# Kernel tuning notes

Hardware: AMD Instinct MI355X
Metric: run time of the kernel (lower is better)

Reference implementation:

```python
import jax, jax.numpy as jnp
import numpy as np

N_EMBD = 126
N_HEADS = 6
HEAD_DIM = N_EMBD // N_HEADS  # 21


def setup_inputs() -> dict:
    key = jax.random.key(0)
    k1, k2, k3 = jax.random.split(key, 3)
    B, T = 8, 2048
    x = jax.random.normal(k1, (B, T, N_EMBD), dtype=jnp.float32)
    # torch Linear weights stored as (out, in); we store transposed (in, out) for x @ W
    w_attn = jax.random.normal(k2, (N_EMBD, 3 * N_EMBD), dtype=jnp.float32) * (1.0 / np.sqrt(N_EMBD))
    w_proj = jax.random.normal(k3, (N_EMBD, N_EMBD), dtype=jnp.float32) * (1.0 / np.sqrt(N_EMBD))
    return {"x": x, "w_attn": w_attn, "w_proj": w_proj}


def reference(x, w_attn, w_proj):
    B, T, C = x.shape
    qkv = x @ w_attn                      # [B, T, 3C]
    q, k, v = jnp.split(qkv, 3, axis=-1)  # each [B, T, C]

    def heads(t):  # [B,T,C] -> [B,H,T,hd]
        return t.reshape(B, T, N_HEADS, HEAD_DIM).transpose(0, 2, 1, 3)

    q, k, v = heads(q), heads(k), heads(v)
    scale = 1.0 / np.sqrt(HEAD_DIM).astype(np.float32)
    scores = jnp.einsum('bhqd,bhkd->bhqk', q, k) * scale  # [B,H,T,T]
    causal = jnp.tril(jnp.ones((T, T), dtype=bool))
    scores = jnp.where(causal, scores, jnp.finfo(scores.dtype).min)
    attn = jax.nn.softmax(scores, axis=-1)
    out = jnp.einsum('bhqk,bhkd->bhqd', attn, v)           # [B,H,T,hd]
    out = out.transpose(0, 2, 1, 3).reshape(B, T, C)
    return out @ w_proj
```

## Files before the change

kernel.cpp:

```cpp
#include <hip/hip_runtime.h>
#include <hip/hip_bf16.h>


#define B_ 8
#define T_ 2048
#define C_ 126
#define H_ 6
#define D_ 21
#define TC_ 378
#define KP_ 128
#define DP_ 32
#define M_ 16384
#define QSCALE 0.31481923469333463f

typedef __hip_bfloat16 bf16;
typedef __bf16 bf16_t;
typedef __bf16 bf16x8 __attribute__((ext_vector_type(8)));
typedef float f32x4 __attribute__((ext_vector_type(4)));

__device__ __forceinline__ float ldf(const bf16* p, long i) { return __bfloat162float(p[i]); }
__device__ __forceinline__ float ldf(const float* p, long i) { return p[i]; }
__device__ __forceinline__ void stf(bf16* p, long i, float v) { p[i] = __float2bfloat16(v); }
__device__ __forceinline__ void stf(float* p, long i, float v) { p[i] = v; }

__device__ __forceinline__ unsigned int ld2(const bf16* x, long i) {
  return *(const unsigned int*)((const unsigned short*)x + i);
}
__device__ __forceinline__ unsigned int ld2(const float* x, long i) {
  const float2 f = *(const float2*)(x + i);
  union { bf16_t b[2]; unsigned int u; } cv;
  cv.b[0] = (bf16_t)f.x; cv.b[1] = (bf16_t)f.y;
  return cv.u;
}

__device__ __forceinline__ void probe_dtype(const void* x, int tid, int* sflag) {
  if (tid < 64) {
    const unsigned int w = ((const unsigned int*)x)[tid * 97 + 13];
    const unsigned int e = (w >> 7) & 0xFF;
    const bool bflike = (e >= 115 && e <= 131) || ((w & 0x7FFFu) == 0);
    const unsigned long long mask = __ballot(bflike);
    if (tid == 0) *sflag = (__popcll(mask) >= 40) ? 1 : 0;
  }
  __syncthreads();
}

template <typename T>
__device__ __forceinline__ void prep_w_body(const T* __restrict__ wa,
                                            const T* __restrict__ wp,
                                            bf16_t* __restrict__ WTa,
                                            bf16_t* __restrict__ WTp) {
  const int stride = gridDim.x * blockDim.x;
  const int idx0 = blockIdx.x * blockDim.x + threadIdx.x;
  for (int i = idx0; i < 384 * KP_ + KP_ * KP_; i += stride) {
    if (i < 384 * KP_) {
      const int n = i >> 7, k = i & 127;
      WTa[i] = (k < C_ && n < TC_) ? (bf16_t)ldf(wa, (long)k * TC_ + n) : (bf16_t)0.f;
    } else {
      const int j = i - 384 * KP_;
      const int n = j >> 7, k = j & 127;
      WTp[j] = (k < C_ && n < C_) ? (bf16_t)ldf(wp, (long)k * C_ + n) : (bf16_t)0.f;
    }
  }
}

__global__ __launch_bounds__(256) void prep_w_kernel(
    const void* __restrict__ x, const void* __restrict__ wa,
    const void* __restrict__ wp, bf16_t* __restrict__ WTa,
    bf16_t* __restrict__ WTp) {
  __shared__ int sflag;
  probe_dtype(x, threadIdx.x, &sflag);
  if (sflag) prep_w_body<bf16>((const bf16*)wa, (const bf16*)wp, WTa, WTp);
  else       prep_w_body<float>((const float*)wa, (const float*)wp, WTa, WTp);
}

#define QS_ 40

template <typename T>
__device__ __forceinline__ void qkv_body(
    const T* __restrict__ x, const bf16_t* __restrict__ WT,
    bf16_t* __restrict__ Qb, bf16_t* __restrict__ Kb, bf16_t* __restrict__ VT,
    bf16_t* __restrict__ xs, bf16_t* __restrict__ qbuf,
    bf16_t* __restrict__ kbuf, bf16_t* __restrict__ vbuf) {
  const int m0 = blockIdx.x * 16;
  const int tid = threadIdx.x;
  for (int i = tid; i < 16 * 64; i += 256) {
    const int row = i >> 6, cp = i & 63;
    unsigned int v = 0;
    if (cp < 63) v = ld2(x, (long)(m0 + row) * C_ + 2 * cp);
    ((unsigned int*)xs)[i] = v;
  }
  for (int i = tid; i < 6 * 16 * 11; i += 256) {
    const int h = i / 176, rem = i - h * 176, t = rem / 11, d = 21 + rem % 11;
    qbuf[(h * 16 + t) * QS_ + d] = (bf16_t)0.f;
    kbuf[(h * 16 + t) * QS_ + d] = (bf16_t)0.f;
  }
  for (int i = tid; i < 6 * 11 * 16; i += 256) {
    const int h = i / 176, rem = i - h * 176, d = 21 + rem / 16, t = rem % 16;
    vbuf[(h * 32 + d) * 16 + t] = (d == 21) ? (bf16_t)1.f : (bf16_t)0.f;
  }
  __syncthreads();

  const int wv = tid >> 6, lane = tid & 63;
  const int lr = lane & 15, quad = lane >> 4;
  const bf16_t* ar = xs + lr * KP_ + quad * 8;
  const bf16x8 a0 = *(const bf16x8*)(ar);
  const bf16x8 a1 = *(const bf16x8*)(ar + 32);
  const bf16x8 a2 = *(const bf16x8*)(ar + 64);
  const bf16x8 a3 = *(const bf16x8*)(ar + 96);

  for (int nt = wv; nt < 24; nt += 4) {
    const int n0 = nt * 16;
    const bf16x8* bp = (const bf16x8*)(WT + (long)(n0 + lr) * KP_ + quad * 8);
    f32x4 acc = {0.f, 0.f, 0.f, 0.f};
    acc = __builtin_amdgcn_mfma_f32_16x16x32_bf16(a0, bp[0],  acc, 0, 0, 0);
    acc = __builtin_amdgcn_mfma_f32_16x16x32_bf16(a1, bp[4],  acc, 0, 0, 0);
    acc = __builtin_amdgcn_mfma_f32_16x16x32_bf16(a2, bp[8],  acc, 0, 0, 0);
    acc = __builtin_amdgcn_mfma_f32_16x16x32_bf16(a3, bp[12], acc, 0, 0, 0);

    const int c = n0 + lr;
    if (c < TC_) {
      const int which = c / C_;
      const int cc = c - which * C_;
      const int h = cc / D_, d = cc - h * D_;
#pragma unroll
      for (int r = 0; r < 4; ++r) {
        const int t = quad * 4 + r;
        if (which == 0)
          qbuf[(h * 16 + t) * QS_ + d] = (bf16_t)(acc[r] * QSCALE);
        else if (which == 1)
          kbuf[(h * 16 + t) * QS_ + d] = (bf16_t)acc[r];
        else
          vbuf[(h * 32 + d) * 16 + t] = (bf16_t)acc[r];
      }
    }
  }
  __syncthreads();

  const int b = m0 >> 11, t0 = m0 & 2047;
  for (int i = tid; i < 192; i += 256) {
    const int j = (i < 96) ? i : i - 96;
    const int h = j >> 4, t = j & 15;
    const int4* src = (const int4*)(((i < 96) ? qbuf : kbuf) + (h * 16 + t) * QS_);
    int4* dst = (int4*)((((i < 96) ? Qb : Kb)) + ((long)(b * H_ + h) * T_ + (t0 + t)) * DP_);
    dst[0] = src[0]; dst[1] = src[1]; dst[2] = src[2]; dst[3] = src[3];
  }
  for (int i = tid; i < 192; i += 256) {
    const int h = i >> 5, d = i & 31;
    const int4* src = (const int4*)(vbuf + (h * 32 + d) * 16);
    int4* dst = (int4*)(VT + ((long)(b * H_ + h) * DP_ + d) * T_ + t0);
    dst[0] = src[0]; dst[1] = src[1];
  }
}

__global__ __launch_bounds__(256) void qkv_mfma(
    const void* __restrict__ x, const bf16_t* __restrict__ WT,
    bf16_t* __restrict__ Qb, bf16_t* __restrict__ Kb, bf16_t* __restrict__ VT) {
  __shared__ __align__(16) bf16_t xs[16 * KP_];
  __shared__ __align__(16) bf16_t qbuf[6 * 16 * QS_];
  __shared__ __align__(16) bf16_t kbuf[6 * 16 * QS_];
  __shared__ __align__(16) bf16_t vbuf[6 * 32 * 16];
  __shared__ int sflag;
  probe_dtype(x, threadIdx.x, &sflag);
  if (sflag) qkv_body<bf16>((const bf16*)x, WT, Qb, Kb, VT, xs, qbuf, kbuf, vbuf);
  else       qkv_body<float>((const float*)x, WT, Qb, Kb, VT, xs, qbuf, kbuf, vbuf);
}

__global__ __launch_bounds__(256, 4) void attn_mfma(
    const bf16_t* __restrict__ Qb, const bf16_t* __restrict__ Kb,
    const bf16_t* __restrict__ VT, bf16_t* __restrict__ ATTp) {
  __shared__ __align__(16) float smem[4352];
  const int bh = blockIdx.x;
  const int pr = 63 - blockIdx.y;
  const int tid = threadIdx.x;
  const int wv = tid >> 6, lane = tid & 63;
  const int lr = lane & 15, quad = lane >> 4;
  const int q0 = pr * 32;
  const int mq = quad * 4;

  const bf16_t* Qbh = Qb + (long)bh * T_ * DP_;
  const bf16_t* Kbh = Kb + (long)bh * T_ * DP_;
  const bf16_t* VTbh = VT + (long)bh * DP_ * T_;

  const bf16x8 qf0 = *(const bf16x8*)(Qbh + (long)(q0 + lr) * DP_ + quad * 8);
  const bf16x8 qf1 = *(const bf16x8*)(Qbh + (long)(q0 + 16 + lr) * DP_ + quad * 8);

  f32x4 o00 = {0.f,0.f,0.f,0.f}, o01 = {0.f,0.f,0.f,0.f};
  f32x4 o10 = {0.f,0.f,0.f,0.f}, o11 = {0.f,0.f,0.f,0.f};
  bf16_t* plA0 = (bf16_t*)smem + wv * 2048;
  bf16_t* plA1 = plA0 + 512;
  bf16_t* plB0 = plA0 + 1024;
  bf16_t* plB1 = plA0 + 1536;
  const int rsw = ((lane ^ (lane >> 2)) << 3);
  const int wb0 = ((lr >> 3) << 4) + mq;

  int t = wv;
  for (; t + 4 <= pr; t += 8) {
    const int kbA = t * 32, kbB = (t + 4) * 32;
    const bf16x8 kA0 = *(const bf16x8*)(Kbh + (long)(kbA + lr) * DP_ + quad * 8);
    const bf16x8 kA1 = *(const bf16x8*)(Kbh + (long)(kbA + 16 + lr) * DP_ + quad * 8);
    const bf16x8 kB0 = *(const bf16x8*)(Kbh + (long)(kbB + lr) * DP_ + quad * 8);
    const bf16x8 kB1 = *(const bf16x8*)(Kbh + (long)(kbB + 16 + lr) * DP_ + quad * 8);
    const bf16x8 vA0 = *(const bf16x8*)(VTbh + (long)lr * T_ + kbA + quad * 8);
    const bf16x8 vA1 = *(const bf16x8*)(VTbh + (long)(16 + lr) * T_ + kbA + quad * 8);
    const bf16x8 vB0 = *(const bf16x8*)(VTbh + (long)lr * T_ + kbB + quad * 8);
    const bf16x8 vB1 = *(const bf16x8*)(VTbh + (long)(16 + lr) * T_ + kbB + quad * 8);

    f32x4 sA00 = {0.f,0.f,0.f,0.f}, sA01 = {0.f,0.f,0.f,0.f};
    f32x4 sA10 = {0.f,0.f,0.f,0.f}, sA11 = {0.f,0.f,0.f,0.f};
    f32x4 sB00 = {0.f,0.f,0.f,0.f}, sB01 = {0.f,0.f,0.f,0.f};
    f32x4 sB10 = {0.f,0.f,0.f,0.f}, sB11 = {0.f,0.f,0.f,0.f};
    sA00 = __builtin_amdgcn_mfma_f32_16x16x32_bf16(qf0, kA0, sA00, 0, 0, 0);
    sA01 = __builtin_amdgcn_mfma_f32_16x16x32_bf16(qf0, kA1, sA01, 0, 0, 0);
    sA10 = __builtin_amdgcn_mfma_f32_16x16x32_bf16(qf1, kA0, sA10, 0, 0, 0);
    sA11 = __builtin_amdgcn_mfma_f32_16x16x32_bf16(qf1, kA1, sA11, 0, 0, 0);
    sB00 = __builtin_amdgcn_mfma_f32_16x16x32_bf16(qf0, kB0, sB00, 0, 0, 0);
    sB01 = __builtin_amdgcn_mfma_f32_16x16x32_bf16(qf0, kB1, sB01, 0, 0, 0);
    sB10 = __builtin_amdgcn_mfma_f32_16x16x32_bf16(qf1, kB0, sB10, 0, 0, 0);
    sB11 = __builtin_amdgcn_mfma_f32_16x16x32_bf16(qf1, kB1, sB11, 0, 0, 0);

    if (t + 4 == pr) {
#pragma unroll
      for (int r = 0; r < 4; ++r) {
        if (lr > mq + r) { sB00[r] = -1e30f; sB11[r] = -1e30f; }
        sB01[r] = -1e30f;
      }
    }
#pragma unroll
    for (int r = 0; r < 4; ++r) {
      const int b0 = wb0 + r, b1 = b0 + 32;
      const int i0 = ((b0 ^ (b0 >> 2)) << 3) + (lr & 7);
      const int i1 = ((b1 ^ (b1 >> 2)) << 3) + (lr & 7);
      plA0[i0] = (bf16_t)exp2f(sA00[r]);
      plA0[i1] = (bf16_t)exp2f(sA01[r]);
      plA1[i0] = (bf16_t)exp2f(sA10[r]);
      plA1[i1] = (bf16_t)exp2f(sA11[r]);
      plB0[i0] = (bf16_t)exp2f(sB00[r]);
      plB0[i1] = (bf16_t)exp2f(sB01[r]);
      plB1[i0] = (bf16_t)exp2f(sB10[r]);
      plB1[i1] = (bf16_t)exp2f(sB11[r]);
    }
    __builtin_amdgcn_wave_barrier();
    const bf16x8 pfA0 = *(const bf16x8*)(plA0 + rsw);
    const bf16x8 pfA1 = *(const bf16x8*)(plA1 + rsw);
    const bf16x8 pfB0 = *(const bf16x8*)(plB0 + rsw);
    const bf16x8 pfB1 = *(const bf16x8*)(plB1 + rsw);
    __builtin_amdgcn_wave_barrier();

    o00 = __builtin_amdgcn_mfma_f32_16x16x32_bf16(pfA0, vA0, o00, 0, 0, 0);
    o01 = __builtin_amdgcn_mfma_f32_16x16x32_bf16(pfA0, vA1, o01, 0, 0, 0);
    o10 = __builtin_amdgcn_mfma_f32_16x16x32_bf16(pfA1, vA0, o10, 0, 0, 0);
    o11 = __builtin_amdgcn_mfma_f32_16x16x32_bf16(pfA1, vA1, o11, 0, 0, 0);
    o00 = __builtin_amdgcn_mfma_f32_16x16x32_bf16(pfB0, vB0, o00, 0, 0, 0);
    o01 = __builtin_amdgcn_mfma_f32_16x16x32_bf16(pfB0, vB1, o01, 0, 0, 0);
    o10 = __builtin_amdgcn_mfma_f32_16x16x32_bf16(pfB1, vB0, o10, 0, 0, 0);
    o11 = __builtin_amdgcn_mfma_f32_16x16x32_bf16(pfB1, vB1, o11, 0, 0, 0);
  }

  if (t <= pr) {
    const int kb = t * 32;
    const bf16x8 k0 = *(const bf16x8*)(Kbh + (long)(kb + lr) * DP_ + quad * 8);
    const bf16x8 k1 = *(const bf16x8*)(Kbh + (long)(kb + 16 + lr) * DP_ + quad * 8);
    const bf16x8 v0 = *(const bf16x8*)(VTbh + (long)lr * T_ + kb + quad * 8);
    const bf16x8 v1 = *(const bf16x8*)(VTbh + (long)(16 + lr) * T_ + kb + quad * 8);
    f32x4 s00 = {0.f,0.f,0.f,0.f}, s01 = {0.f,0.f,0.f,0.f};
    f32x4 s10 = {0.f,0.f,0.f,0.f}, s11 = {0.f,0.f,0.f,0.f};
    s00 = __builtin_amdgcn_mfma_f32_16x16x32_bf16(qf0, k0, s00, 0, 0, 0);
    s01 = __builtin_amdgcn_mfma_f32_16x16x32_bf16(qf0, k1, s01, 0, 0, 0);
    s10 = __builtin_amdgcn_mfma_f32_16x16x32_bf16(qf1, k0, s10, 0, 0, 0);
    s11 = __builtin_amdgcn_mfma_f32_16x16x32_bf16(qf1, k1, s11, 0, 0, 0);
    if (t == pr) {
#pragma unroll
      for (int r = 0; r < 4; ++r) {
        if (lr > mq + r) { s00[r] = -1e30f; s11[r] = -1e30f; }
        s01[r] = -1e30f;
      }
    }
#pragma unroll
    for (int r = 0; r < 4; ++r) {
      const int b0 = wb0 + r, b1 = b0 + 32;
      const int i0 = ((b0 ^ (b0 >> 2)) << 3) + (lr & 7);
      const int i1 = ((b1 ^ (b1 >> 2)) << 3) + (lr & 7);
      plA0[i0] = (bf16_t)exp2f(s00[r]);
      plA0[i1] = (bf16_t)exp2f(s01[r]);
      plA1[i0] = (bf16_t)exp2f(s10[r]);
      plA1[i1] = (bf16_t)exp2f(s11[r]);
    }
    __builtin_amdgcn_wave_barrier();
    const bf16x8 pf0 = *(const bf16x8*)(plA0 + rsw);
    const bf16x8 pf1 = *(const bf16x8*)(plA1 + rsw);
    __builtin_amdgcn_wave_barrier();
    o00 = __builtin_amdgcn_mfma_f32_16x16x32_bf16(pf0, v0, o00, 0, 0, 0);
    o01 = __builtin_amdgcn_mfma_f32_16x16x32_bf16(pf0, v1, o01, 0, 0, 0);
    o10 = __builtin_amdgcn_mfma_f32_16x16x32_bf16(pf1, v0, o10, 0, 0, 0);
    o11 = __builtin_amdgcn_mfma_f32_16x16x32_bf16(pf1, v1, o11, 0, 0, 0);
  }

  __syncthreads();
  {
    float* my = smem + (wv * 64 + lane) * 17;
#pragma unroll
    for (int j = 0; j < 4; ++j) {
      my[j]      = o00[j];
      my[4 + j]  = o01[j];
      my[8 + j]  = o10[j];
      my[12 + j] = o11[j];
    }
  }
  __syncthreads();

  if (wv == 0) {
    float tot[16];
#pragma unroll
    for (int j = 0; j < 16; ++j)
      tot[j] = smem[lane * 17 + j] + smem[(64 + lane) * 17 + j] +
               smem[(128 + lane) * 17 + j] + smem[(192 + lane) * 17 + j];
    const int b = bh / H_, h = bh - b * H_;
#pragma unroll
    for (int r = 0; r < 4; ++r) {
      const float rl0 = 1.f / __shfl(tot[4 + r],  (lane & 48) + 5, 64);
      const float rl1 = 1.f / __shfl(tot[12 + r], (lane & 48) + 5, 64);
      const int qA = q0 + mq + r, qB = qA + 16;
      bf16_t* opA = ATTp + (long)(b * T_ + qA) * KP_ + h * D_;
      bf16_t* opB = ATTp + (long)(b * T_ + qB) * KP_ + h * D_;
      opA[lr] = (bf16_t)(tot[r] * rl0);
      opB[lr] = (bf16_t)(tot[8 + r] * rl1);
      if (lr < 5) {
        opA[16 + lr] = (bf16_t)(tot[4 + r] * rl0);
        opB[16 + lr] = (bf16_t)(tot[12 + r] * rl1);
      }
    }
  }
}

__global__ __launch_bounds__(256) void proj_mfma(
    const void* __restrict__ x, const bf16_t* __restrict__ ATTp,
    const bf16_t* __restrict__ WT, void* __restrict__ out) {
  __shared__ int sflag;
  probe_dtype(x, threadIdx.x, &sflag);
  const int isbf = sflag;

  const int m0 = blockIdx.x * 16;
  const int tid = threadIdx.x;
  const int wv = tid >> 6, lane = tid & 63;
  const int lr = lane & 15, quad = lane >> 4;

  const bf16x8* ap = (const bf16x8*)(ATTp + (long)(m0 + lr) * KP_ + quad * 8);
  const bf16x8 a0 = ap[0], a1 = ap[4], a2 = ap[8], a3 = ap[12];

  for (int nt = wv; nt < 8; nt += 4) {
    const int n0 = nt * 16;
    const bf16x8* bp = (const bf16x8*)(WT + (long)(n0 + lr) * KP_ + quad * 8);
    f32x4 acc = {0.f, 0.f, 0.f, 0.f};
    acc = __builtin_amdgcn_mfma_f32_16x16x32_bf16(a0, bp[0],  acc, 0, 0, 0);
    acc = __builtin_amdgcn_mfma_f32_16x16x32_bf16(a1, bp[4],  acc, 0, 0, 0);
    acc = __builtin_amdgcn_mfma_f32_16x16x32_bf16(a2, bp[8],  acc, 0, 0, 0);
    acc = __builtin_amdgcn_mfma_f32_16x16x32_bf16(a3, bp[12], acc, 0, 0, 0);

    const int c = n0 + lr;
    if (c < C_) {
#pragma unroll
      for (int r = 0; r < 4; ++r) {
        const int m = m0 + quad * 4 + r;
        if (isbf) stf((bf16*)out,  (long)m * C_ + c, acc[r]);
        else      stf((float*)out, (long)m * C_ + c, acc[r]);
      }
    }
  }
}

extern "C" void kernel_launch(void* const* d_in, const int* in_sizes, int n_in,
                              void* d_out, int out_size, void* d_ws, size_t ws_size,
                              hipStream_t stream) {
  const void* x      = d_in[0];
  const void* w_attn = d_in[1];
  const void* w_proj = d_in[2];

  char* base = (char*)d_ws;
  const long QKV = (long)48 * T_ * DP_;
  bf16_t* Qb = (bf16_t*)(base + 256);
  bf16_t* Kb = Qb + QKV;
  bf16_t* VT = Kb + QKV;
  bf16_t* WTa  = VT + QKV;
  bf16_t* WTp  = WTa + 384 * KP_;
  bf16_t* ATTp = WTp + KP_ * KP_;

  prep_w_kernel<<<64, 256, 0, stream>>>(x, w_attn, w_proj, WTa, WTp);
  qkv_mfma<<<M_ / 16, 256, 0, stream>>>(x, WTa, Qb, Kb, VT);
  attn_mfma<<<dim3(48, 64), 256, 0, stream>>>(Qb, Kb, VT, ATTp);
  proj_mfma<<<M_ / 16, 256, 0, stream>>>(x, ATTp, WTp, d_out);
}
```

Baseline: 135.5 us.

## Build P fragments in registers via permlane swaps instead of LDS round-trip

```diff
diff --git a/kernel.cpp b/kernel.cpp
--- a/kernel.cpp
+++ b/kernel.cpp
@@ -15,8 +15,10 @@
 
 typedef __hip_bfloat16 bf16;
 typedef __bf16 bf16_t;
+typedef __bf16 bf16x2 __attribute__((ext_vector_type(2)));
 typedef __bf16 bf16x8 __attribute__((ext_vector_type(8)));
 typedef float f32x4 __attribute__((ext_vector_type(4)));
+typedef int int2v __attribute__((ext_vector_type(2)));
 
 __device__ __forceinline__ float ldf(const bf16* p, long i) { return __bfloat162float(p[i]); }
 __device__ __forceinline__ float ldf(const float* p, long i) { return p[i]; }
@@ -165,6 +167,48 @@
   else       qkv_body<float>((const float*)x, WT, Qb, Kb, VT, xs, qbuf, kbuf, vbuf);
 }
 
+__device__ __forceinline__ void swap32(int& a, int& b) {
+#if __has_builtin(__builtin_amdgcn_permlane32_swap)
+  const int2v r = __builtin_amdgcn_permlane32_swap(a, b, false, false);
+  a = r[0]; b = r[1];
+#else
+  const int sa = __shfl_xor(a, 32, 64), sb = __shfl_xor(b, 32, 64);
+  const bool hi = (threadIdx.x & 32) != 0;
+  a = hi ? sb : a;
+  b = hi ? b : sa;
+#endif
+}
+
+__device__ __forceinline__ void swap16(int& a, int& b) {
+#if __has_builtin(__builtin_amdgcn_permlane16_swap)
+  const int2v r = __builtin_amdgcn_permlane16_swap(a, b, false, false);
+  a = r[0]; b = r[1];
+#else
+  const int sa = __shfl_xor(a, 16, 64), sb = __shfl_xor(b, 16, 64);
+  const bool odd = (threadIdx.x & 16) != 0;
+  a = odd ? sb : a;
+  b = odd ? b : sa;
+#endif
+}
+
+__device__ __forceinline__ int pkbf(float x, float y) {
+  union { bf16x2 h; int i; } u;
+  u.h[0] = (bf16_t)x; u.h[1] = (bf16_t)y;
+  return u.i;
+}
+
+__device__ __forceinline__ bf16x8 build_frag(const f32x4 g1, const f32x4 g2) {
+  int a1 = pkbf(g1[0], g1[1]);
+  int b1 = pkbf(g1[2], g1[3]);
+  int a2 = pkbf(g2[0], g2[1]);
+  int b2 = pkbf(g2[2], g2[3]);
+  swap32(a1, a2); swap32(b1, b2);
+  swap16(a1, a2); swap16(b1, b2);
+  union { int i[4]; bf16x8 v; } u;
+  u.i[0] = a1; u.i[1] = b1; u.i[2] = a2; u.i[3] = b2;
+  return u.v;
+}
+
 __global__ __launch_bounds__(256, 4) void attn_mfma(
     const bf16_t* __restrict__ Qb, const bf16_t* __restrict__ Kb,
     const bf16_t* __restrict__ VT, bf16_t* __restrict__ ATTp) {
@@ -186,12 +230,6 @@
 
   f32x4 o00 = {0.f,0.f,0.f,0.f}, o01 = {0.f,0.f,0.f,0.f};
   f32x4 o10 = {0.f,0.f,0.f,0.f}, o11 = {0.f,0.f,0.f,0.f};
-  bf16_t* plA0 = (bf16_t*)smem + wv * 2048;
-  bf16_t* plA1 = plA0 + 512;
-  bf16_t* plB0 = plA0 + 1024;
-  bf16_t* plB1 = plA0 + 1536;
-  const int rsw = ((lane ^ (lane >> 2)) << 3);
-  const int wb0 = ((lr >> 3) << 4) + mq;
 
   int t = wv;
   for (; t + 4 <= pr; t += 8) {
@@ -209,51 +247,42 @@
     f32x4 sA10 = {0.f,0.f,0.f,0.f}, sA11 = {0.f,0.f,0.f,0.f};
     f32x4 sB00 = {0.f,0.f,0.f,0.f}, sB01 = {0.f,0.f,0.f,0.f};
     f32x4 sB10 = {0.f,0.f,0.f,0.f}, sB11 = {0.f,0.f,0.f,0.f};
-    sA00 = __builtin_amdgcn_mfma_f32_16x16x32_bf16(qf0, kA0, sA00, 0, 0, 0);
-    sA01 = __builtin_amdgcn_mfma_f32_16x16x32_bf16(qf0, kA1, sA01, 0, 0, 0);
-    sA10 = __builtin_amdgcn_mfma_f32_16x16x32_bf16(qf1, kA0, sA10, 0, 0, 0);
-    sA11 = __builtin_amdgcn_mfma_f32_16x16x32_bf16(qf1, kA1, sA11, 0, 0, 0);
-    sB00 = __builtin_amdgcn_mfma_f32_16x16x32_bf16(qf0, kB0, sB00, 0, 0, 0);
-    sB01 = __builtin_amdgcn_mfma_f32_16x16x32_bf16(qf0, kB1, sB01, 0, 0, 0);
-    sB10 = __builtin_amdgcn_mfma_f32_16x16x32_bf16(qf1, kB0, sB10, 0, 0, 0);
-    sB11 = __builtin_amdgcn_mfma_f32_16x16x32_bf16(qf1, kB1, sB11, 0, 0, 0);
+    sA00 = __builtin_amdgcn_mfma_f32_16x16x32_bf16(kA0, qf0, sA00, 0, 0, 0);
+    sA01 = __builtin_amdgcn_mfma_f32_16x16x32_bf16(kA0, qf1, sA01, 0, 0, 0);
+    sA10 = __builtin_amdgcn_mfma_f32_16x16x32_bf16(kA1, qf0, sA10, 0, 0, 0);
+    sA11 = __builtin_amdgcn_mfma_f32_16x16x32_bf16(kA1, qf1, sA11, 0, 0, 0);
+    sB00 = __builtin_amdgcn_mfma_f32_16x16x32_bf16(kB0, qf0, sB00, 0, 0, 0);
+    sB01 = __builtin_amdgcn_mfma_f32_16x16x32_bf16(kB0, qf1, sB01, 0, 0, 0);
+    sB10 = __builtin_amdgcn_mfma_f32_16x16x32_bf16(kB1, qf0, sB10, 0, 0, 0);
+    sB11 = __builtin_amdgcn_mfma_f32_16x16x32_bf16(kB1, qf1, sB11, 0, 0, 0);
 
     if (t + 4 == pr) {
 #pragma unroll
       for (int r = 0; r < 4; ++r) {
-        if (lr > mq + r) { sB00[r] = -1e30f; sB11[r] = -1e30f; }
-        sB01[r] = -1e30f;
+        if (mq + r > lr) { sB00[r] = -1e30f; sB11[r] = -1e30f; }
+        sB10[r] = -1e30f;
       }
     }
 #pragma unroll
     for (int r = 0; r < 4; ++r) {
-      const int b0 = wb0 + r, b1 = b0 + 32;
-      const int i0 = ((b0 ^ (b0 >> 2)) << 3) + (lr & 7);
-      const int i1 = ((b1 ^ (b1 >> 2)) << 3) + (lr & 7);
-      plA0[i0] = (bf16_t)exp2f(sA00[r]);
-      plA0[i1] = (bf16_t)exp2f(sA01[r]);
-      plA1[i0] = (bf16_t)exp2f(sA10[r]);
-      plA1[i1] = (bf16_t)exp2f(sA11[r]);
-      plB0[i0] = (bf16_t)exp2f(sB00[r]);
-      plB0[i1] = (bf16_t)exp2f(sB01[r]);
-      plB1[i0] = (bf16_t)exp2f(sB10[r]);
-      plB1[i1] = (bf16_t)exp2f(sB11[r]);
-    }
-    __builtin_amdgcn_wave_barrier();
-    const bf16x8 pfA0 = *(const bf16x8*)(plA0 + rsw);
-    const bf16x8 pfA1 = *(const bf16x8*)(plA1 + rsw);
-    const bf16x8 pfB0 = *(const bf16x8*)(plB0 + rsw);
-    const bf16x8 pfB1 = *(const bf16x8*)(plB1 + rsw);
-    __builtin_amdgcn_wave_barrier();
-
-    o00 = __builtin_amdgcn_mfma_f32_16x16x32_bf16(pfA0, vA0, o00, 0, 0, 0);
-    o01 = __builtin_amdgcn_mfma_f32_16x16x32_bf16(pfA0, vA1, o01, 0, 0, 0);
-    o10 = __builtin_amdgcn_mfma_f32_16x16x32_bf16(pfA1, vA0, o10, 0, 0, 0);
-    o11 = __builtin_amdgcn_mfma_f32_16x16x32_bf16(pfA1, vA1, o11, 0, 0, 0);
-    o00 = __builtin_amdgcn_mfma_f32_16x16x32_bf16(pfB0, vB0, o00, 0, 0, 0);
-    o01 = __builtin_amdgcn_mfma_f32_16x16x32_bf16(pfB0, vB1, o01, 0, 0, 0);
-    o10 = __builtin_amdgcn_mfma_f32_16x16x32_bf16(pfB1, vB0, o10, 0, 0, 0);
-    o11 = __builtin_amdgcn_mfma_f32_16x16x32_bf16(pfB1, vB1, o11, 0, 0, 0);
+      sA00[r] = exp2f(sA00[r]); sA01[r] = exp2f(sA01[r]);
+      sA10[r] = exp2f(sA10[r]); sA11[r] = exp2f(sA11[r]);
+      sB00[r] = exp2f(sB00[r]); sB01[r] = exp2f(sB01[r]);
+      sB10[r] = exp2f(sB10[r]); sB11[r] = exp2f(sB11[r]);
+    }
+    const bf16x8 pA0 = build_frag(sA00, sA10);
+    const bf16x8 pA1 = build_frag(sA01, sA11);
+    const bf16x8 pB0 = build_frag(sB00, sB10);
+    const bf16x8 pB1 = build_frag(sB01, sB11);
+
+    o00 = __builtin_amdgcn_mfma_f32_16x16x32_bf16(pA0, vA0, o00, 0, 0, 0);
+    o01 = __builtin_amdgcn_mfma_f32_16x16x32_bf16(pA0, vA1, o01, 0, 0, 0);
+    o10 = __builtin_amdgcn_mfma_f32_16x16x32_bf16(pA1, vA0, o10, 0, 0, 0);
+    o11 = __builtin_amdgcn_mfma_f32_16x16x32_bf16(pA1, vA1, o11, 0, 0, 0);
+    o00 = __builtin_amdgcn_mfma_f32_16x16x32_bf16(pB0, vB0, o00, 0, 0, 0);
+    o01 = __builtin_amdgcn_mfma_f32_16x16x32_bf16(pB0, vB1, o01, 0, 0, 0);
+    o10 = __builtin_amdgcn_mfma_f32_16x16x32_bf16(pB1, vB0, o10, 0, 0, 0);
+    o11 = __builtin_amdgcn_mfma_f32_16x16x32_bf16(pB1, vB1, o11, 0, 0, 0);
   }
 
   if (t <= pr) {
@@ -264,31 +293,24 @@
     const bf16x8 v1 = *(const bf16x8*)(VTbh + (long)(16 + lr) * T_ + kb + quad * 8);
     f32x4 s00 = {0.f,0.f,0.f,0.f}, s01 = {0.f,0.f,0.f,0.f};
     f32x4 s10 = {0.f,0.f,0.f,0.f}, s11 = {0.f,0.f,0.f,0.f};
-    s00 = __builtin_amdgcn_mfma_f32_16x16x32_bf16(qf0, k0, s00, 0, 0, 0);
-    s01 = __builtin_amdgcn_mfma_f32_16x16x32_bf16(qf0, k1, s01, 0, 0, 0);
-    s10 = __builtin_amdgcn_mfma_f32_16x16x32_bf16(qf1, k0, s10, 0, 0, 0);
-    s11 = __builtin_amdgcn_mfma_f32_16x16x32_bf16(qf1, k1, s11, 0, 0, 0);
+    s00 = __builtin_amdgcn_mfma_f32_16x16x32_bf16(k0, qf0, s00, 0, 0, 0);
+    s01 = __builtin_amdgcn_mfma_f32_16x16x32_bf16(k0, qf1, s01, 0, 0, 0);
+    s10 = __builtin_amdgcn_mfma_f32_16x16x32_bf16(k1, qf0, s10, 0, 0, 0);
+    s11 = __builtin_amdgcn_mfma_f32_16x16x32_bf16(k1, qf1, s11, 0, 0, 0);
     if (t == pr) {
 #pragma unroll
       for (int r = 0; r < 4; ++r) {
-        if (lr > mq + r) { s00[r] = -1e30f; s11[r] = -1e30f; }
-        s01[r] = -1e30f;
+        if (mq + r > lr) { s00[r] = -1e30f; s11[r] = -1e30f; }
+        s10[r] = -1e30f;
       }
     }
 #pragma unroll
     for (int r = 0; r < 4; ++r) {
-      const int b0 = wb0 + r, b1 = b0 + 32;
-      const int i0 = ((b0 ^ (b0 >> 2)) << 3) + (lr & 7);
-      const int i1 = ((b1 ^ (b1 >> 2)) << 3) + (lr & 7);
-      plA0[i0] = (bf16_t)exp2f(s00[r]);
-      plA0[i1] = (bf16_t)exp2f(s01[r]);
-      plA1[i0] = (bf16_t)exp2f(s10[r]);
-      plA1[i1] = (bf16_t)exp2f(s11[r]);
-    }
-    __builtin_amdgcn_wave_barrier();
-    const bf16x8 pf0 = *(const bf16x8*)(plA0 + rsw);
-    const bf16x8 pf1 = *(const bf16x8*)(plA1 + rsw);
-    __builtin_amdgcn_wave_barrier();
+      s00[r] = exp2f(s00[r]); s01[r] = exp2f(s01[r]);
+      s10[r] = exp2f(s10[r]); s11[r] = exp2f(s11[r]);
+    }
+    const bf16x8 pf0 = build_frag(s00, s10);
+    const bf16x8 pf1 = build_frag(s01, s11);
     o00 = __builtin_amdgcn_mfma_f32_16x16x32_bf16(pf0, v0, o00, 0, 0, 0);
     o01 = __builtin_amdgcn_mfma_f32_16x16x32_bf16(pf0, v1, o01, 0, 0, 0);
     o10 = __builtin_amdgcn_mfma_f32_16x16x32_bf16(pf1, v0, o10, 0, 0, 0);
```

Result: faster. 132.4 us (-2.3%).
